# Optimization experiments

Measured on AMD Instinct MI355X. Metric: run time of the kernel, lower is better.

## Reference

```python
import jax, jax.numpy as jnp
import numpy as np

KERNEL = 11  # matches AttnBlock(kernel_size=11)
EPS = 1e-4


def _patches(x, k):
    """Extract k x k patches (stride 1, VALID), matching nn.Unfold ordering.

    x: [B, C, H, W] -> ([B, L, C*k*k], (Hp, Wp)) with L = Hp*Wp.
    """
    p = jax.lax.conv_general_dilated_patches(x, (k, k), (1, 1), 'VALID')  # [B, C*k*k, Hp, Wp]
    B, D, Hp, Wp = p.shape
    return p.reshape(B, D, Hp * Wp).transpose(0, 2, 1), (Hp, Wp)


def setup_inputs() -> dict:
    key = jax.random.key(0)
    k1, k2 = jax.random.split(key)
    im1 = jax.random.normal(k1, (4, 64, 40, 40), dtype=jnp.float32)
    im2 = jax.random.normal(k2, (4, 64, 40, 40), dtype=jnp.float32)
    return {"im1": im1, "im2": im2}


def reference(im1, im2):
    k = KERNEL
    # Dynamic per-sample filters from im1 patches, L2-normalized per patch.
    p1, _ = _patches(im1, k)                                  # [B, L, D], D = C*k*k
    norm = jnp.sqrt(jnp.sum(p1 * p1, axis=-1, keepdims=True))  # [B, L, 1]
    p1n = p1 / jnp.maximum(norm, EPS)
    # conv2d(im2, filters) with stride 1 / no padding == dot of im2 patches with filters.
    p2, (Hp, Wp) = _patches(im2, k)                           # [B, P, D], P = Hp*Wp
    scores = jnp.einsum('bld,bpd->bpl', p1n, p2)              # [B, P, L]
    out = jnp.max(scores, axis=-1)                            # max over filter (channel) dim
    B = im1.shape[0]
    return out.reshape(B, 1, Hp, Wp)
```

## Files before the change

### kernel.cpp

```cpp
#include <hip/hip_runtime.h>

#define C_    64
#define H_    40
#define W_    40
#define KS    11
#define HP    30
#define NB    4
#define NL    900
#define ND    59
#define EPSF  1e-4f
#define PCH   6
#define SCW   65
#define NINF  -3.4e38f
#define MPAD  1664
#define GSTEP 66600

typedef _Float16 f16x8 __attribute__((ext_vector_type(8)));
typedef float    f32x4 __attribute__((ext_vector_type(4)));

__global__ __launch_bounds__(128)
void k_pack(const float* __restrict__ im2, const float* __restrict__ im1,
            _Float16* __restrict__ packed, float* __restrict__ ssqbuf,
            unsigned int* __restrict__ keys) {
    const int blk = blockIdx.x, b = blockIdx.y, img = blockIdx.z;
    const int pos = blk * 128 + threadIdx.x;
    const float* src = (img ? im1 : im2) + b * C_ * 1600;
    _Float16* dst = packed + ((size_t)img * NB + b) * (8 * MPAD * 8);
    float ss = 0.f;
    #pragma unroll
    for (int oct = 0; oct < 8; ++oct) {
        f16x8 h = {};
        if (pos < 1600) {
            #pragma unroll
            for (int j = 0; j < 8; ++j) {
                float v = src[(oct * 8 + j) * 1600 + pos];
                h[j] = (_Float16)v;
                ss += v * v;
            }
        }
        *(f16x8*)&dst[(oct * MPAD + pos) * 8] = h;
    }
    if (img == 1 && pos < 1600) ssqbuf[b * 1600 + pos] = ss;
    if (img == 0 && pos < NL) keys[b * NL + pos] = 0u;
}

__global__ __launch_bounds__(1024)
void k_norm(const float* __restrict__ ssqbuf, float* __restrict__ invnorm) {
    const int b = blockIdx.x, tid = threadIdx.x;
    __shared__ float ssq[1600];
    __shared__ float colsum[1200];
    for (int i = tid; i < 1600; i += 1024) ssq[i] = ssqbuf[b * 1600 + i];
    __syncthreads();
    for (int t = tid; t < HP * W_; t += 1024) {
        int yy = t / W_, x = t - yy * W_;
        float s = 0.f;
        #pragma unroll
        for (int r = 0; r < KS; ++r) s += ssq[(yy + r) * W_ + x];
        colsum[t] = s;
    }
    __syncthreads();
    for (int t = tid; t < NL; t += 1024) {
        int ly = t / HP, lx = t - ly * HP;
        float s = 0.f;
        #pragma unroll
        for (int sx = 0; sx < KS; ++sx) s += colsum[ly * W_ + lx + sx];
        invnorm[b * NL + t] = 1.f / fmaxf(sqrtf(s), EPSF);
    }
}

__global__ __launch_bounds__(256, 3)
void k_gram(const _Float16* __restrict__ packed, _Float16* __restrict__ G) {
    const int i = blockIdx.x, j = blockIdx.y, b = blockIdx.z;
    int dd = i - j; if (dd < 0) dd = -dd;
    if (dd > 10) return;
    const int tid = threadIdx.x;
    const int w = tid >> 6, L = tid & 63, lq = L >> 4, lr = L & 15;

    __shared__ __align__(16) _Float16 smem[128 * 136];
    _Float16 (*As)[128][8] = (_Float16 (*)[128][8])smem;
    _Float16 (*Bs)[128][8] = (_Float16 (*)[128][8])(smem + 8192);

    const _Float16* pa = packed + (size_t)b * (8 * MPAD * 8);
    const _Float16* pb = packed + (size_t)(NB + b) * (8 * MPAD * 8);
    for (int t = tid; t < 1024; t += 256) {
        int oct = t >> 7, m = t & 127;
        *(f16x8*)&As[oct][m][0] = *(const f16x8*)&pa[(oct * MPAD + i * 128 + m) * 8];
        *(f16x8*)&Bs[oct][m][0] = *(const f16x8*)&pb[(oct * MPAD + j * 128 + m) * 8];
    }
    __syncthreads();

    const int mb = (w & 1) * 64, nb = (w >> 1) * 64;
    f16x8 a0[4], a1[4], b0[4], b1[4];
    #pragma unroll
    for (int q = 0; q < 4; ++q) {
        a0[q] = *(const f16x8*)&As[lq][mb + q * 16 + lr][0];
        a1[q] = *(const f16x8*)&As[4 + lq][mb + q * 16 + lr][0];
        b0[q] = *(const f16x8*)&Bs[lq][nb + q * 16 + lr][0];
        b1[q] = *(const f16x8*)&Bs[4 + lq][nb + q * 16 + lr][0];
    }
    f32x4 acc[4][4];
    #pragma unroll
    for (int mi = 0; mi < 4; ++mi)
        #pragma unroll
        for (int ni = 0; ni < 4; ++ni) {
            f32x4 c = {0.f, 0.f, 0.f, 0.f};
            c = __builtin_amdgcn_mfma_f32_16x16x32_f16(a0[mi], b0[ni], c, 0, 0, 0);
            c = __builtin_amdgcn_mfma_f32_16x16x32_f16(a1[mi], b1[ni], c, 0, 0, 0);
            acc[mi][ni] = c;
        }
    __syncthreads();
    #pragma unroll
    for (int mi = 0; mi < 4; ++mi)
        #pragma unroll
        for (int ni = 0; ni < 4; ++ni)
            #pragma unroll
            for (int rg = 0; rg < 4; ++rg)
                smem[(mb + mi * 16 + lq * 4 + rg) * 136 + nb + ni * 16 + lr] =
                    (_Float16)acc[mi][ni][rg];
    __syncthreads();
    _Float16* Gb = G + (size_t)b * (MPAD * MPAD);
    for (int t = tid; t < 2048; t += 256) {
        int row = t >> 4, seg = t & 15;
        *(f16x8*)&Gb[(size_t)(i * 128 + row) * MPAD + j * 128 + seg * 8] =
            *(const f16x8*)&smem[row * 136 + seg * 8];
    }
}

__global__ __launch_bounds__(256, 4)
void k_box(const _Float16* __restrict__ G, const float* __restrict__ invnorm,
           unsigned int* __restrict__ keys) {
    const int chunk = blockIdx.x;
    const int dy = (int)blockIdx.y - (HP - 1);
    const int b = blockIdx.z;
    const int ady = dy < 0 ? -dy : dy;
    const int rows = HP - ady;
    if (chunk * PCH >= rows) return;
    const int pyLo = dy < 0 ? -dy : 0;
    const int py0 = pyLo + chunk * PCH;
    const int P = min(PCH, rows - chunk * PCH);
    const int tid = threadIdx.x;

    __shared__ float csum[1600];
    __shared__ float scratch[HP * SCW];
    __shared__ float partials[120];
    __shared__ float sInvAll[PCH][HP];

    if (tid < P * HP) {
        int i = tid / HP, lx = tid - i * HP;
        sInvAll[i][lx] = invnorm[b * NL + (py0 + i + dy) * HP + lx];
    }

    const _Float16* Gb = G + (size_t)b * (MPAD * MPAD);
    float s[8];
    f16x8 qa, qs;
    const _Float16* base = nullptr;
    if (tid < 200) {
        int e = tid * 8, x2 = e / 40, x1 = e - x2 * 40;
        base = Gb + (size_t)py0 * GSTEP + x2 * MPAD + dy * 40 + x1;
        #pragma unroll
        for (int j = 0; j < 8; ++j) s[j] = 0.f;
        for (int r = 0; r < KS; ++r) {
            f16x8 q = *(const f16x8*)(base + r * GSTEP);
            #pragma unroll
            for (int j = 0; j < 8; ++j) s[j] += (float)q[j];
        }
    }

    for (int i = 0; i < P; ++i) {
        const int py = py0 + i;
        if (tid < 200) {
            if (i > 0) {
                #pragma unroll
                for (int j = 0; j < 8; ++j) s[j] += (float)qa[j] - (float)qs[j];
            }
            float4* c4 = (float4*)(csum + tid * 8);
            c4[0] = make_float4(s[0], s[1], s[2], s[3]);
            c4[1] = make_float4(s[4], s[5], s[6], s[7]);
            if (i + 1 < P) {
                qa = *(const f16x8*)(base + (i + 11) * GSTEP);
                qs = *(const f16x8*)(base + i * GSTEP);
            }
        }
        __syncthreads();
        for (int t = tid; t < 5 * ND; t += 256) {
            int pg = t / ND, dxI = t - ND * pg;
            int dx = dxI - (HP - 1), pxb = 6 * pg;
            #pragma unroll
            for (int u = 0; u < 6; ++u) scratch[(pxb + u) * SCW + dxI] = NINF;
            int u0 = max(0, -dx - pxb), u1 = min(5, (HP - 1) - dx - pxb);
            if (u0 <= u1) {
                const float* cp = csum + dx;
                float run = 0.f;
                #pragma unroll
                for (int sr = 0; sr < KS; ++sr) run += cp[(pxb + u0 + sr) * (W_ + 1)];
                int u = u0;
                for (;;) {
                    scratch[(pxb + u) * SCW + dxI] = run * sInvAll[i][pxb + u + dx];
                    if (++u > u1) break;
                    run += cp[(pxb + u + 10) * (W_ + 1)] - cp[(pxb + u - 1) * (W_ + 1)];
                }
            }
        }
        __syncthreads();
        if (tid < 120) {
            int px = tid >> 2, q = tid & 3;
            float m = NINF;
            int d0 = q * 15, d1 = min(d0 + 15, ND);
            for (int d = d0; d < d1; ++d) m = fmaxf(m, scratch[px * SCW + d]);
            partials[tid] = m;
        }
        __syncthreads();
        if (tid < HP) {
            float m = fmaxf(fmaxf(partials[tid * 4], partials[tid * 4 + 1]),
                            fmaxf(partials[tid * 4 + 2], partials[tid * 4 + 3]));
            unsigned int ub = __float_as_uint(m);
            unsigned int k = (ub & 0x80000000u) ? ~ub : (ub | 0x80000000u);
            atomicMax(&keys[b * NL + py * HP + tid], k);
        }
    }
}

__global__ __launch_bounds__(256)
void k_decode(const unsigned int* __restrict__ keys, float* __restrict__ out) {
    int i = blockIdx.x * 256 + threadIdx.x;
    if (i < NB * NL) {
        unsigned int k = keys[i];
        unsigned int u = (k & 0x80000000u) ? (k ^ 0x80000000u) : ~k;
        out[i] = __uint_as_float(u);
    }
}

__global__ __launch_bounds__(256)
void k_norm_fb(const float* __restrict__ im1, float* __restrict__ invnorm) {
    const int ly = blockIdx.x, b = blockIdx.y;
    const int tid = threadIdx.x;
    __shared__ float colsq[KS * W_];
    __shared__ float colsum[W_];
    const float* base = im1 + b * C_ * H_ * W_;
    for (int i = tid; i < KS * W_; i += 256) {
        int r = i / W_, x = i - r * W_;
        const float* p = base + (ly + r) * W_ + x;
        float s = 0.f;
        #pragma unroll 8
        for (int c = 0; c < C_; ++c) { float v = p[c * H_ * W_]; s += v * v; }
        colsq[i] = s;
    }
    __syncthreads();
    if (tid < W_) {
        float s = 0.f;
        #pragma unroll
        for (int r = 0; r < KS; ++r) s += colsq[r * W_ + tid];
        colsum[tid] = s;
    }
    __syncthreads();
    if (tid < HP) {
        float s = 0.f;
        #pragma unroll
        for (int sx = 0; sx < KS; ++sx) s += colsum[tid + sx];
        invnorm[b * NL + ly * HP + tid] = 1.f / fmaxf(sqrtf(s), EPSF);
    }
}

#define MAXPL 16
__global__ __launch_bounds__(256, 2)
void k_main_fb(const float* __restrict__ im1, const float* __restrict__ im2,
               const float* __restrict__ invnorm, unsigned int* __restrict__ keys) {
    const int chunk = blockIdx.x;
    const int dy = (int)blockIdx.y - (HP - 1);
    const int b = blockIdx.z;
    const int ady = dy < 0 ? -dy : dy;
    const int rows = HP - ady;
    if (chunk * PCH >= rows) return;
    const int pyLo = dy < 0 ? -dy : 0;
    const int py0 = pyLo + chunk * PCH;
    const int P = min(PCH, rows - chunk * PCH);
    const int nPl = P + KS - 1;
    const int tid = threadIdx.x;
    const int w = tid >> 6, L = tid & 63, lq = L >> 4, lr = L & 15;

    __shared__ __align__(16) _Float16 planes[MAXPL][H_ * W_];
    __shared__ __align__(16) float csum[H_ * W_];
    __shared__ __align__(16) _Float16 Astg[8][48][8];
    __shared__ __align__(16) _Float16 Bstg[8][48][8];
    __shared__ float scratch[HP * SCW];
    __shared__ float partials[120];
    __shared__ float sInv[HP];

    const float* im1b = im1 + b * C_ * H_ * W_;
    const float* im2b = im2 + b * C_ * H_ * W_;
    if (tid < 128) {
        int arr = tid >> 6, r = tid & 63;
        int oct = r >> 3, x = 40 + (r & 7);
        f16x8 z = {};
        *(f16x8*)((arr ? Bstg : Astg)[oct][x]) = z;
    }
    for (int p = 0; p < nPl; ++p) {
        const int y = py0 + p;
        for (int t = tid; t < 640; t += 256) {
            int arr = t >= 320;
            int r = arr ? t - 320 : t;
            int oct = r / 40, x = r - oct * 40;
            const float* pc = (arr ? (im1b + (y + dy) * W_) : (im2b + y * W_))
                              + oct * 8 * H_ * W_ + x;
            f16x8 h;
            #pragma unroll
            for (int j = 0; j < 8; ++j) h[j] = (_Float16)pc[j * H_ * W_];
            *(f16x8*)((arr ? Bstg : Astg)[oct][x]) = h;
        }
        __syncthreads();
        for (int t = w; t < 9; t += 4) {
            int mt = t / 3, nt = t - 3 * mt;
            f16x8 a0 = *(const f16x8*)(Astg[lq][mt * 16 + lr]);
            f16x8 b0 = *(const f16x8*)(Bstg[lq][nt * 16 + lr]);
            f16x8 a1 = *(const f16x8*)(Astg[4 + lq][mt * 16 + lr]);
            f16x8 b1 = *(const f16x8*)(Bstg[4 + lq][nt * 16 + lr]);
            f32x4 acc = {0.f, 0.f, 0.f, 0.f};
            acc = __builtin_amdgcn_mfma_f32_16x16x32_f16(a0, b0, acc, 0, 0, 0);
            acc = __builtin_amdgcn_mfma_f32_16x16x32_f16(a1, b1, acc, 0, 0, 0);
            int x1 = nt * 16 + lr;
            if (x1 < W_) {
                int x2b = mt * 16 + lq * 4;
                #pragma unroll
                for (int rg = 0; rg < 4; ++rg) {
                    int x2 = x2b + rg;
                    if (x2 < W_) planes[p][x2 * W_ + x1] = (_Float16)acc[rg];
                }
            }
        }
        __syncthreads();
    }
    for (int i = 0; i < P; ++i) {
        const int py = py0 + i, ly = py + dy;
        if (tid < 200) {
            float4* c4 = (float4*)(csum + tid * 8);
            if (i == 0) {
                float s[8] = {0.f,0.f,0.f,0.f,0.f,0.f,0.f,0.f};
                #pragma unroll
                for (int r = 0; r < KS; ++r) {
                    f16x8 q = *(const f16x8*)(planes[r] + tid * 8);
                    #pragma unroll
                    for (int j = 0; j < 8; ++j) s[j] += (float)q[j];
                }
                c4[0] = make_float4(s[0], s[1], s[2], s[3]);
                c4[1] = make_float4(s[4], s[5], s[6], s[7]);
            } else {
                f16x8 qa = *(const f16x8*)(planes[i + 10] + tid * 8);
                f16x8 qs = *(const f16x8*)(planes[i - 1] + tid * 8);
                float4 v0 = c4[0], v1 = c4[1];
                v0.x += (float)qa[0] - (float)qs[0]; v0.y += (float)qa[1] - (float)qs[1];
                v0.z += (float)qa[2] - (float)qs[2]; v0.w += (float)qa[3] - (float)qs[3];
                v1.x += (float)qa[4] - (float)qs[4]; v1.y += (float)qa[5] - (float)qs[5];
                v1.z += (float)qa[6] - (float)qs[6]; v1.w += (float)qa[7] - (float)qs[7];
                c4[0] = v0; c4[1] = v1;
            }
        } else if (tid >= 224 && tid < 224 + HP) {
            sInv[tid - 224] = invnorm[b * NL + ly * HP + (tid - 224)];
        }
        __syncthreads();
        for (int t = tid; t < 5 * ND; t += 256) {
            int pg = t / ND, dxI = t - ND * pg;
            int dx = dxI - (HP - 1), pxb = 6 * pg;
            #pragma unroll
            for (int u = 0; u < 6; ++u) scratch[(pxb + u) * SCW + dxI] = NINF;
            int u0 = max(0, -dx - pxb), u1 = min(5, (HP - 1) - dx - pxb);
            if (u0 <= u1) {
                const float* cp = csum + dx;
                float run = 0.f;
                #pragma unroll
                for (int sr = 0; sr < KS; ++sr) run += cp[(pxb + u0 + sr) * (W_ + 1)];
                int u = u0;
                for (;;) {
                    scratch[(pxb + u) * SCW + dxI] = run * sInv[pxb + u + dx];
                    if (++u > u1) break;
                    run += cp[(pxb + u + 10) * (W_ + 1)] - cp[(pxb + u - 1) * (W_ + 1)];
                }
            }
        }
        __syncthreads();
        if (tid < 120) {
            int px = tid >> 2, q = tid & 3;
            float m = NINF;
            int d0 = q * 15, d1 = min(d0 + 15, ND);
            for (int d = d0; d < d1; ++d) m = fmaxf(m, scratch[px * SCW + d]);
            partials[tid] = m;
        }
        __syncthreads();
        if (tid < HP) {
            float m = fmaxf(fmaxf(partials[tid * 4], partials[tid * 4 + 1]),
                            fmaxf(partials[tid * 4 + 2], partials[tid * 4 + 3]));
            unsigned int ub = __float_as_uint(m);
            unsigned int k = (ub & 0x80000000u) ? ~ub : (ub | 0x80000000u);
            atomicMax(&keys[b * NL + py * HP + tid], k);
        }
        __syncthreads();
    }
}

extern "C" void kernel_launch(void* const* d_in, const int* in_sizes, int n_in,
                              void* d_out, int out_size, void* d_ws, size_t ws_size,
                              hipStream_t stream) {
    const float* im1 = (const float*)d_in[0];
    const float* im2 = (const float*)d_in[1];
    unsigned int* keys = (unsigned int*)d_ws;
    float* invnorm = (float*)((char*)d_ws + 14400);
    float* ssqbuf  = (float*)((char*)d_ws + 28800);
    const size_t packedOff = 65536;
    const size_t packedBytes = (size_t)2 * NB * 8 * MPAD * 8 * 2;
    const size_t gOff = packedOff + packedBytes;
    const size_t gBytes = (size_t)NB * MPAD * MPAD * 2;
    const size_t needed = gOff + gBytes;

    if (ws_size >= needed) {
        _Float16* packed = (_Float16*)((char*)d_ws + packedOff);
        _Float16* G = (_Float16*)((char*)d_ws + gOff);
        k_pack<<<dim3(13, NB, 2), 128, 0, stream>>>(im2, im1, packed, ssqbuf, keys);
        k_norm<<<NB, 1024, 0, stream>>>(ssqbuf, invnorm);
        k_gram<<<dim3(13, 13, NB), 256, 0, stream>>>(packed, G);
        k_box<<<dim3(5, ND, NB), 256, 0, stream>>>(G, invnorm, keys);
    } else {
        hipMemsetAsync(d_ws, 0, NB * NL * sizeof(unsigned int), stream);
        k_norm_fb<<<dim3(HP, NB), 256, 0, stream>>>(im1, invnorm);
        k_main_fb<<<dim3(5, ND, NB), 256, 0, stream>>>(im1, im2, invnorm, keys);
    }
    k_decode<<<(NB * NL + 255) / 256, 256, 0, stream>>>(keys, (float*)d_out);
}
```

Before: 102.7 us.

## Fold norm kernel into idle gram blocks and reindex box max by filter x

The separate k_norm launch is removed. Its inverse-norm computation now runs in k_gram blocks that would otherwise exit early because they lie outside the band, with three such blocks per batch each covering ten filter rows. In k_box, scratch is indexed by filter column instead of dx, which removes the per-column NINF fill. The inverse norm is applied during the max, and a two-stage reduction with an extra sync is replaced by 8-lane shuffles. This saves a kernel launch and some shared-memory traffic, at the cost of a somewhat more intricate indexing scheme.

```diff
diff --git a/kernel.cpp b/kernel.cpp
--- a/kernel.cpp
+++ b/kernel.cpp
@@ -11,6 +11,7 @@
 #define EPSF  1e-4f
 #define PCH   6
 #define SCW   65
+#define SCB   33
 #define NINF  -3.4e38f
 #define MPAD  1664
 #define GSTEP 66600
@@ -44,39 +45,43 @@
     if (img == 0 && pos < NL) keys[b * NL + pos] = 0u;
 }
 
-__global__ __launch_bounds__(1024)
-void k_norm(const float* __restrict__ ssqbuf, float* __restrict__ invnorm) {
-    const int b = blockIdx.x, tid = threadIdx.x;
-    __shared__ float ssq[1600];
-    __shared__ float colsum[1200];
-    for (int i = tid; i < 1600; i += 1024) ssq[i] = ssqbuf[b * 1600 + i];
-    __syncthreads();
-    for (int t = tid; t < HP * W_; t += 1024) {
-        int yy = t / W_, x = t - yy * W_;
-        float s = 0.f;
-        #pragma unroll
-        for (int r = 0; r < KS; ++r) s += ssq[(yy + r) * W_ + x];
-        colsum[t] = s;
-    }
-    __syncthreads();
-    for (int t = tid; t < NL; t += 1024) {
-        int ly = t / HP, lx = t - ly * HP;
-        float s = 0.f;
-        #pragma unroll
-        for (int sx = 0; sx < KS; ++sx) s += colsum[ly * W_ + lx + sx];
-        invnorm[b * NL + t] = 1.f / fmaxf(sqrtf(s), EPSF);
-    }
-}
-
 __global__ __launch_bounds__(256, 3)
-void k_gram(const _Float16* __restrict__ packed, _Float16* __restrict__ G) {
+void k_gram(const _Float16* __restrict__ packed, _Float16* __restrict__ G,
+            const float* __restrict__ ssqbuf, float* __restrict__ invnorm) {
     const int i = blockIdx.x, j = blockIdx.y, b = blockIdx.z;
+    const int tid = threadIdx.x;
+    __shared__ __align__(16) _Float16 smem[128 * 136];
+
     int dd = i - j; if (dd < 0) dd = -dd;
-    if (dd > 10) return;
-    const int tid = threadIdx.x;
+    if (dd > 10) {
+        if (i < j) {
+            const int part = (j == 11) ? 0 : ((i == 0) ? 1 : 2);
+            const int ly0 = part * 10;
+            float* ssq = (float*)smem;
+            float* colsum = ssq + 800;
+            for (int t = tid; t < 800; t += 256)
+                ssq[t] = ssqbuf[b * 1600 + ly0 * W_ + t];
+            __syncthreads();
+            for (int t = tid; t < 10 * W_; t += 256) {
+                int yy = t / W_, x = t - yy * W_;
+                float s = 0.f;
+                #pragma unroll
+                for (int r = 0; r < KS; ++r) s += ssq[(yy + r) * W_ + x];
+                colsum[t] = s;
+            }
+            __syncthreads();
+            for (int t = tid; t < 10 * HP; t += 256) {
+                int ly = t / HP, lx = t - ly * HP;
+                float s = 0.f;
+                #pragma unroll
+                for (int sx = 0; sx < KS; ++sx) s += colsum[ly * W_ + lx + sx];
+                invnorm[b * NL + (ly0 + ly) * HP + lx] = 1.f / fmaxf(sqrtf(s), EPSF);
+            }
+        }
+        return;
+    }
     const int w = tid >> 6, L = tid & 63, lq = L >> 4, lr = L & 15;
 
-    __shared__ __align__(16) _Float16 smem[128 * 136];
     _Float16 (*As)[128][8] = (_Float16 (*)[128][8])smem;
     _Float16 (*Bs)[128][8] = (_Float16 (*)[128][8])(smem + 8192);
 
@@ -141,8 +146,7 @@
     const int tid = threadIdx.x;
 
     __shared__ float csum[1600];
-    __shared__ float scratch[HP * SCW];
-    __shared__ float partials[120];
+    __shared__ float scratch[HP * SCB];
     __shared__ float sInvAll[PCH][HP];
 
     if (tid < P * HP) {
@@ -185,8 +189,6 @@
         for (int t = tid; t < 5 * ND; t += 256) {
             int pg = t / ND, dxI = t - ND * pg;
             int dx = dxI - (HP - 1), pxb = 6 * pg;
-            #pragma unroll
-            for (int u = 0; u < 6; ++u) scratch[(pxb + u) * SCW + dxI] = NINF;
             int u0 = max(0, -dx - pxb), u1 = min(5, (HP - 1) - dx - pxb);
             if (u0 <= u1) {
                 const float* cp = csum + dx;
@@ -195,27 +197,32 @@
                 for (int sr = 0; sr < KS; ++sr) run += cp[(pxb + u0 + sr) * (W_ + 1)];
                 int u = u0;
                 for (;;) {
-                    scratch[(pxb + u) * SCW + dxI] = run * sInvAll[i][pxb + u + dx];
+                    int px = pxb + u;
+                    scratch[px * SCB + px + dx] = run;
                     if (++u > u1) break;
                     run += cp[(pxb + u + 10) * (W_ + 1)] - cp[(pxb + u - 1) * (W_ + 1)];
                 }
             }
         }
         __syncthreads();
-        if (tid < 120) {
-            int px = tid >> 2, q = tid & 3;
+        if (tid < 240) {
+            int px = tid >> 3, l = tid & 7;
+            const float* srow = scratch + px * SCB;
+            const float* inv = sInvAll[i];
             float m = NINF;
-            int d0 = q * 15, d1 = min(d0 + 15, ND);
-            for (int d = d0; d < d1; ++d) m = fmaxf(m, scratch[px * SCW + d]);
-            partials[tid] = m;
-        }
-        __syncthreads();
-        if (tid < HP) {
-            float m = fmaxf(fmaxf(partials[tid * 4], partials[tid * 4 + 1]),
-                            fmaxf(partials[tid * 4 + 2], partials[tid * 4 + 3]));
-            unsigned int ub = __float_as_uint(m);
-            unsigned int k = (ub & 0x80000000u) ? ~ub : (ub | 0x80000000u);
-            atomicMax(&keys[b * NL + py * HP + tid], k);
+            #pragma unroll
+            for (int k = 0; k < 4; ++k) {
+                int lx = l + 8 * k;
+                if (lx < HP) m = fmaxf(m, srow[lx] * inv[lx]);
+            }
+            m = fmaxf(m, __shfl_xor(m, 1));
+            m = fmaxf(m, __shfl_xor(m, 2));
+            m = fmaxf(m, __shfl_xor(m, 4));
+            if (l == 0) {
+                unsigned int ub = __float_as_uint(m);
+                unsigned int k = (ub & 0x80000000u) ? ~ub : (ub | 0x80000000u);
+                atomicMax(&keys[b * NL + py * HP + px], k);
+            }
         }
     }
 }
@@ -414,8 +421,7 @@
         _Float16* packed = (_Float16*)((char*)d_ws + packedOff);
         _Float16* G = (_Float16*)((char*)d_ws + gOff);
         k_pack<<<dim3(13, NB, 2), 128, 0, stream>>>(im2, im1, packed, ssqbuf, keys);
-        k_norm<<<NB, 1024, 0, stream>>>(ssqbuf, invnorm);
-        k_gram<<<dim3(13, 13, NB), 256, 0, stream>>>(packed, G);
+        k_gram<<<dim3(13, 13, NB), 256, 0, stream>>>(packed, G, ssqbuf, invnorm);
         k_box<<<dim3(5, ND, NB), 256, 0, stream>>>(G, invnorm, keys);
     } else {
         hipMemsetAsync(d_ws, 0, NB * NL * sizeof(unsigned int), stream);
```

Result: faster. 98.26 us (-4.3%).
